# Optimization experiments

Measured on AMD Instinct MI355X. Metric: run time of the kernel, lower is better.

Reference implementation:

```python
import jax, jax.numpy as jnp
import numpy as np

N_NODES = 4096
EDGE_PROB = 0.01


def setup_inputs() -> dict:
    key = jax.random.key(0)
    kx, ka, kw = jax.random.split(key, 3)
    x = jax.random.normal(kx, (4, 32, N_NODES, 12), dtype=jnp.float32)
    u = jax.random.uniform(ka, (N_NODES, N_NODES), dtype=jnp.float32)
    adj = (u < EDGE_PROB).astype(jnp.float32)
    adj = jnp.maximum(adj, adj.T)
    weight = jax.random.normal(kw, (3, 32, 32), dtype=jnp.float32) * 0.1
    bias = jnp.zeros((32,), dtype=jnp.float32)
    return {"x": x, "adj": adj, "weight": weight, "bias": bias}


def reference(x, adj, weight, bias):
    # x: [B, c_in, N, T] -> [B, T, N, c_in] as in AdaptiveGraphConv.forward
    B, C, N, T = x.shape
    h = jnp.transpose(x, (0, 3, 2, 1))  # [B, T, N, C]
    # DenseChebConv (K=3): L = I - D^{-1/2} A D^{-1/2}, inf -> 0 for isolated nodes
    d = adj.sum(axis=-1)
    d_inv_sqrt = jnp.where(d > 0, jnp.where(d > 0, d, 1.0) ** -0.5, 0.0)
    norm_adj = d_inv_sqrt[:, None] * adj * d_inv_sqrt[None, :]
    L = jnp.eye(N, dtype=x.dtype) - norm_adj
    Tx0 = h
    Tx1 = jnp.einsum('mn,btnc->btmc', L, h)
    Tx2 = 2.0 * jnp.einsum('mn,btnc->btmc', L, Tx1) - Tx0
    out = (jnp.einsum('btnc,co->btno', Tx0, weight[0])
           + jnp.einsum('btnc,co->btno', Tx1, weight[1])
           + jnp.einsum('btnc,co->btno', Tx2, weight[2])
           + bias)
    # back to [B, c_out, N, T]
    return jnp.transpose(out, (0, 3, 2, 1))
```

## Files before the change

### kernel.cpp

```cpp
#include <hip/hip_runtime.h>

#define NN 4096
#define CC 32
#define TT 12
#define BB 4
#define BT 48
#define NC 1536
#define MAXD 192
#define FW 256
#define NCH 6
#define SOP 33

typedef float f32x4 __attribute__((ext_vector_type(4)));
typedef short short8 __attribute__((ext_vector_type(8)));

__device__ __forceinline__ float bf2f(unsigned short h) {
  return __uint_as_float(((unsigned int)h) << 16);
}
__device__ __forceinline__ unsigned short f2bf(float f) {
  unsigned int u = __float_as_uint(f);
  return (unsigned short)((u + 0x7FFFu + ((u >> 16) & 1u)) >> 16);
}
__device__ __forceinline__ float blo(unsigned int w) { return __uint_as_float(w << 16); }
__device__ __forceinline__ float bhi(unsigned int w) { return __uint_as_float(w & 0xFFFF0000u); }

__global__ void k_detect(const unsigned int* __restrict__ w, int* __restrict__ flag) {
  __shared__ int s;
  if (threadIdx.x == 0) s = 0;
  __syncthreads();
  int h = 0;
  for (int i = threadIdx.x; i < 256; i += 64) {
    unsigned int e = (w[i] >> 7) & 0xFFu;
    if (e >= 90u && e <= 141u) ++h;
  }
  atomicAdd(&s, h);
  __syncthreads();
  if (threadIdx.x == 0) *flag = (s >= 150) ? 1 : 0;
}

template<int BF16>
__global__ __launch_bounds__(256) void k_build(const void* __restrict__ adjv,
                                               uint2* __restrict__ edges,
                                               int* __restrict__ deg, float* __restrict__ dis,
                                               const int* __restrict__ flag) {
  if ((*flag != 0) != (BF16 != 0)) return;
  __shared__ int cnt;
  int m = blockIdx.x;
  if (threadIdx.x == 0) cnt = 0;
  __syncthreads();
  unsigned int* ecol = (unsigned int*)(edges + m * MAXD);
  if (BF16) {
    const uint4* row = (const uint4*)((const unsigned short*)adjv + (size_t)m * NN);
    for (int i = threadIdx.x; i < NN / 8; i += 256) {
      uint4 v = row[i];
      unsigned int ws[4] = {v.x, v.y, v.z, v.w};
      #pragma unroll
      for (int k = 0; k < 4; ++k) {
        if (ws[k] & 0xFFFFu) {
          int p = atomicAdd(&cnt, 1);
          if (p < MAXD) ecol[p * 2] = (unsigned int)(i * 8 + k * 2);
        }
        if (ws[k] >> 16) {
          int p = atomicAdd(&cnt, 1);
          if (p < MAXD) ecol[p * 2] = (unsigned int)(i * 8 + k * 2 + 1);
        }
      }
    }
  } else {
    const uint4* row = (const uint4*)((const float*)adjv + (size_t)m * NN);
    for (int i = threadIdx.x; i < NN / 4; i += 256) {
      uint4 v = row[i];
      unsigned int ws[4] = {v.x, v.y, v.z, v.w};
      #pragma unroll
      for (int k = 0; k < 4; ++k) {
        if (ws[k] != 0) {
          int p = atomicAdd(&cnt, 1);
          if (p < MAXD) ecol[p * 2] = (unsigned int)(i * 4 + k);
        }
      }
    }
  }
  __syncthreads();
  if (threadIdx.x == 0) {
    int d = cnt < MAXD ? cnt : MAXD;
    deg[m] = d;
    dis[m] = d > 0 ? (float)(1.0 / sqrt((double)d)) : 0.0f;
  }
}

__global__ __launch_bounds__(192) void k_wt(uint2* __restrict__ edges,
                                            const int* __restrict__ deg,
                                            const float* __restrict__ dis) {
  int m = blockIdx.x;
  int j = threadIdx.x;
  if (j < deg[m]) {
    unsigned int* e = (unsigned int*)(edges + m * MAXD + j);
    unsigned int col = e[0];
    e[1] = __float_as_uint(dis[col]);
  }
}

template<int BF16>
__global__ __launch_bounds__(256) void k_trans(const void* __restrict__ xv,
                                               unsigned short* __restrict__ H,
                                               const int* __restrict__ flag) {
  if ((*flag != 0) != (BF16 != 0)) return;
  int i = blockIdx.x * 256 + threadIdx.x;
  int c4 = (i & 7) << 2;
  int r  = i >> 3;
  int bt = r % BT;
  int b  = bt / TT;
  int t  = bt - b * TT;
  int n  = r / BT;
  const size_t S = (size_t)NN * TT;
  size_t src = ((((size_t)b * CC + c4) * NN + n) * TT + t);
  ushort4 v;
  if (BF16) {
    const unsigned short* x = (const unsigned short*)xv;
    v.x = x[src]; v.y = x[src + S]; v.z = x[src + 2 * S]; v.w = x[src + 3 * S];
  } else {
    const float* x = (const float*)xv;
    v.x = f2bf(x[src]); v.y = f2bf(x[src + S]);
    v.z = f2bf(x[src + 2 * S]); v.w = f2bf(x[src + 3 * S]);
  }
  *(ushort4*)(H + (size_t)r * CC + c4) = v;
}

__global__ __launch_bounds__(256) void k_gather1(const unsigned short* __restrict__ H,
                                                 const uint2* __restrict__ edges,
                                                 const int* __restrict__ deg,
                                                 const float* __restrict__ dis,
                                                 unsigned short* __restrict__ T1) {
  int wid = __builtin_amdgcn_readfirstlane(threadIdx.x >> 6);
  int lane = threadIdx.x & 63;
  int m = blockIdx.x * 4 + wid;
  int q = blockIdx.y;
  int d = deg[m];
  float dm = dis[m];
  const uint2* ep = edges + m * MAXD;
  int fo = q * FW + (lane << 2);
  const unsigned short* Hf = H + fo;
  float a0 = 0.f, a1 = 0.f, a2 = 0.f, a3 = 0.f;
  #pragma unroll 4
  for (int e = 0; e < d; ++e) {
    uint2 ew = ep[e];
    int cc = (int)ew.x;
    float w = __uint_as_float(ew.y);
    uint2 hv = *(const uint2*)(Hf + cc * NC);
    a0 = fmaf(w, blo(hv.x), a0);
    a1 = fmaf(w, bhi(hv.x), a1);
    a2 = fmaf(w, blo(hv.y), a2);
    a3 = fmaf(w, bhi(hv.y), a3);
  }
  uint2 hm = *(const uint2*)(Hf + m * NC);
  ushort4 o;
  o.x = f2bf(blo(hm.x) - dm * a0);
  o.y = f2bf(bhi(hm.x) - dm * a1);
  o.z = f2bf(blo(hm.y) - dm * a2);
  o.w = f2bf(bhi(hm.y) - dm * a3);
  *(ushort4*)(T1 + (size_t)m * NC + fo) = o;
}

__global__ __launch_bounds__(256) void k_gather2(const unsigned short* __restrict__ H,
                                                 const unsigned short* __restrict__ T1,
                                                 const uint2* __restrict__ edges,
                                                 const int* __restrict__ deg,
                                                 const float* __restrict__ dis,
                                                 unsigned short* __restrict__ T2) {
  int wid = __builtin_amdgcn_readfirstlane(threadIdx.x >> 6);
  int lane = threadIdx.x & 63;
  int m = blockIdx.x * 4 + wid;
  int q = blockIdx.y;
  int d = deg[m];
  float dm = dis[m];
  const uint2* ep = edges + m * MAXD;
  int fo = q * FW + (lane << 2);
  const unsigned short* Tf = T1 + fo;
  float a0 = 0.f, a1 = 0.f, a2 = 0.f, a3 = 0.f;
  #pragma unroll 4
  for (int e = 0; e < d; ++e) {
    uint2 ew = ep[e];
    int cc = (int)ew.x;
    float w = __uint_as_float(ew.y);
    uint2 hv = *(const uint2*)(Tf + cc * NC);
    a0 = fmaf(w, blo(hv.x), a0);
    a1 = fmaf(w, bhi(hv.x), a1);
    a2 = fmaf(w, blo(hv.y), a2);
    a3 = fmaf(w, bhi(hv.y), a3);
  }
  uint2 tm = *(const uint2*)(Tf + m * NC);
  uint2 hm = *(const uint2*)(H + (size_t)m * NC + fo);
  float td = 2.f * dm;
  ushort4 o;
  o.x = f2bf(2.f * blo(tm.x) - td * a0 - blo(hm.x));
  o.y = f2bf(2.f * bhi(tm.x) - td * a1 - bhi(hm.x));
  o.z = f2bf(2.f * blo(tm.y) - td * a2 - blo(hm.y));
  o.w = f2bf(2.f * bhi(tm.y) - td * a3 - bhi(hm.y));
  *(ushort4*)(T2 + (size_t)m * NC + fo) = o;
}

template<int BF16>
__global__ __launch_bounds__(256) void k_mix(const unsigned short* __restrict__ H,
                                             const unsigned short* __restrict__ T1,
                                             const unsigned short* __restrict__ T2,
                                             const void* __restrict__ wgtv,
                                             const void* __restrict__ biasv,
                                             void* __restrict__ outv,
                                             const int* __restrict__ flag) {
  if ((*flag != 0) != (BF16 != 0)) return;
  __shared__ __align__(16) float sOut[192 * SOP];
  int wid = threadIdx.x >> 6, lane = threadIdx.x & 63;
  int lm = lane & 15, quad = lane >> 4;
  short8 bhf[2][3], blf[2][3];
  for (int h = 0; h < 2; ++h) {
    for (int g = 0; g < 3; ++g) {
      short8 vh, vl;
      #pragma unroll
      for (int j = 0; j < 8; ++j) {
        int c = quad * 8 + j;
        int o = h * 16 + lm;
        float w = BF16 ? bf2f(((const unsigned short*)wgtv)[(g * CC + c) * CC + o])
                       : ((const float*)wgtv)[(g * CC + c) * CC + o];
        unsigned short hi = f2bf(w);
        float rem = w - bf2f(hi);
        vh[j] = (short)hi;
        vl[j] = (short)f2bf(rem);
      }
      bhf[h][g] = vh;
      blf[h][g] = vl;
    }
  }
  float bias0[2];
  #pragma unroll
  for (int h = 0; h < 2; ++h) {
    bias0[h] = BF16 ? bf2f(((const unsigned short*)biasv)[h * 16 + lm])
                    : ((const float*)biasv)[h * 16 + lm];
  }
  int n0 = blockIdx.x * 4;
  #pragma unroll
  for (int tI = 0; tI < 3; ++tI) {
    int r0l = wid * BT + tI * 16;
    size_t abase = ((size_t)(n0 * BT) + r0l + lm) * CC + quad * 8;
    short8 af0 = *(const short8*)(H + abase);
    short8 af1 = *(const short8*)(T1 + abase);
    short8 af2 = *(const short8*)(T2 + abase);
    #pragma unroll
    for (int h = 0; h < 2; ++h) {
      f32x4 acc = {bias0[h], bias0[h], bias0[h], bias0[h]};
      acc = __builtin_amdgcn_mfma_f32_16x16x32_bf16(af0, bhf[h][0], acc, 0, 0, 0);
      acc = __builtin_amdgcn_mfma_f32_16x16x32_bf16(af0, blf[h][0], acc, 0, 0, 0);
      acc = __builtin_amdgcn_mfma_f32_16x16x32_bf16(af1, bhf[h][1], acc, 0, 0, 0);
      acc = __builtin_amdgcn_mfma_f32_16x16x32_bf16(af1, blf[h][1], acc, 0, 0, 0);
      acc = __builtin_amdgcn_mfma_f32_16x16x32_bf16(af2, bhf[h][2], acc, 0, 0, 0);
      acc = __builtin_amdgcn_mfma_f32_16x16x32_bf16(af2, blf[h][2], acc, 0, 0, 0);
      int o = h * 16 + lm;
      #pragma unroll
      for (int reg = 0; reg < 4; ++reg) {
        sOut[(r0l + quad * 4 + reg) * SOP + o] = acc[reg];
      }
    }
  }
  __syncthreads();
  #pragma unroll
  for (int j = 0; j < 6; ++j) {
    int idx = j * 256 + threadIdx.x;
    int bo = idx / 12;
    int fq = idx - bo * 12;
    int b = bo >> 5, o = bo & 31;
    int p0 = fq * 4;
    float v[4];
    #pragma unroll
    for (int k = 0; k < 4; ++k) {
      int p = p0 + k;
      int nl = p / 12, t = p - nl * 12;
      v[k] = sOut[(nl * BT + b * TT + t) * SOP + o];
    }
    size_t base = (((size_t)bo * NN) + n0) * TT + p0;
    if (BF16) {
      ushort4 s = {f2bf(v[0]), f2bf(v[1]), f2bf(v[2]), f2bf(v[3])};
      *(ushort4*)((unsigned short*)outv + base) = s;
    } else {
      *(float4*)((float*)outv + base) = make_float4(v[0], v[1], v[2], v[3]);
    }
  }
}

extern "C" void kernel_launch(void* const* d_in, const int* in_sizes, int n_in,
                              void* d_out, int out_size, void* d_ws, size_t ws_size,
                              hipStream_t stream) {
  const void* x    = d_in[0];
  const void* adj  = d_in[1];
  const void* wgt  = d_in[2];
  const void* bias = d_in[3];
  char* ws = (char*)d_ws;
  int*   flag = (int*)ws;
  float* dis  = (float*)(ws + 256);
  int*   deg  = (int*)(ws + 256 + 16384);
  uint2* edges = (uint2*)(ws + 256 + 32768);
  char* p = ws + 256 + 32768 + (size_t)NN * MAXD * 8;
  unsigned short* H  = (unsigned short*)p;
  unsigned short* T1 = (unsigned short*)(p + (size_t)NN * NC * 2);
  unsigned short* T2 = (unsigned short*)(p + (size_t)NN * NC * 4);

  k_detect<<<1, 64, 0, stream>>>((const unsigned int*)wgt, flag);
  k_build<1><<<NN, 256, 0, stream>>>(adj, edges, deg, dis, flag);
  k_build<0><<<NN, 256, 0, stream>>>(adj, edges, deg, dis, flag);
  k_wt<<<NN, 192, 0, stream>>>(edges, deg, dis);
  k_trans<1><<<(NN * BT * 8) / 256, 256, 0, stream>>>(x, H, flag);
  k_trans<0><<<(NN * BT * 8) / 256, 256, 0, stream>>>(x, H, flag);
  k_gather1<<<dim3(NN / 4, NCH), 256, 0, stream>>>(H, edges, deg, dis, T1);
  k_gather2<<<dim3(NN / 4, NCH), 256, 0, stream>>>(H, T1, edges, deg, dis, T2);
  k_mix<1><<<NN / 4, 256, 0, stream>>>(H, T1, T2, wgt, bias, d_out, flag);
  k_mix<0><<<NN / 4, 256, 0, stream>>>(H, T1, T2, wgt, bias, d_out, flag);
}
```

Baseline: 285.9 us.

## Inline dtype sniffing, tile transpose via LDS, widen gather vectors, pad edge lists

Removes the separate dtype-detect kernel and the duplicated templated launches by having each kernel sniff the weight dtype itself. The input transpose is reworked to use an LDS tile, so global reads are coalesced vector loads instead of strided scalar ones. The gathers now load 8 bf16 per lane (16-byte loads) with half as many feature chunks. Edge lists are padded to a multiple of 8 with zero-weight self edges so the unrolled loop has no remainder. The cost is redundant sniffing work in every block and more registers per thread in the gathers.

```diff
diff --git a/kernel.cpp b/kernel.cpp
--- a/kernel.cpp
+++ b/kernel.cpp
@@ -7,9 +7,9 @@
 #define BT 48
 #define NC 1536
 #define MAXD 192
-#define FW 256
-#define NCH 6
-#define SOP 33
+#define FWW 512
+#define NCH 3
+#define STP 36
 
 typedef float f32x4 __attribute__((ext_vector_type(4)));
 typedef short short8 __attribute__((ext_vector_type(8)));
@@ -24,32 +24,28 @@
 __device__ __forceinline__ float blo(unsigned int w) { return __uint_as_float(w << 16); }
 __device__ __forceinline__ float bhi(unsigned int w) { return __uint_as_float(w & 0xFFFF0000u); }
 
-__global__ void k_detect(const unsigned int* __restrict__ w, int* __restrict__ flag) {
-  __shared__ int s;
-  if (threadIdx.x == 0) s = 0;
-  __syncthreads();
-  int h = 0;
-  for (int i = threadIdx.x; i < 256; i += 64) {
-    unsigned int e = (w[i] >> 7) & 0xFFu;
-    if (e >= 90u && e <= 141u) ++h;
-  }
-  atomicAdd(&s, h);
-  __syncthreads();
-  if (threadIdx.x == 0) *flag = (s >= 150) ? 1 : 0;
-}
-
-template<int BF16>
+__device__ __forceinline__ int sniff_bf16(const void* w) {
+  const unsigned int* p = (const unsigned int*)w;
+  int hits = 0;
+  #pragma unroll 8
+  for (int i = 0; i < 256; ++i) {
+    unsigned int e = (p[i] >> 7) & 0xFFu;
+    hits += (e >= 90u && e <= 141u) ? 1 : 0;
+  }
+  return hits >= 150;
+}
+
 __global__ __launch_bounds__(256) void k_build(const void* __restrict__ adjv,
+                                               const void* __restrict__ wgtv,
                                                uint2* __restrict__ edges,
-                                               int* __restrict__ deg, float* __restrict__ dis,
-                                               const int* __restrict__ flag) {
-  if ((*flag != 0) != (BF16 != 0)) return;
+                                               int* __restrict__ deg, float* __restrict__ dis) {
+  int bf16 = sniff_bf16(wgtv);
   __shared__ int cnt;
   int m = blockIdx.x;
   if (threadIdx.x == 0) cnt = 0;
   __syncthreads();
   unsigned int* ecol = (unsigned int*)(edges + m * MAXD);
-  if (BF16) {
+  if (bf16) {
     const uint4* row = (const uint4*)((const unsigned short*)adjv + (size_t)m * NN);
     for (int i = threadIdx.x; i < NN / 8; i += 256) {
       uint4 v = row[i];
@@ -89,41 +85,56 @@
 }
 
 __global__ __launch_bounds__(192) void k_wt(uint2* __restrict__ edges,
-                                            const int* __restrict__ deg,
+                                            int* __restrict__ deg,
                                             const float* __restrict__ dis) {
   int m = blockIdx.x;
   int j = threadIdx.x;
-  if (j < deg[m]) {
+  int d = deg[m];
+  int dp = (d + 7) & ~7;
+  if (j < d) {
     unsigned int* e = (unsigned int*)(edges + m * MAXD + j);
-    unsigned int col = e[0];
-    e[1] = __float_as_uint(dis[col]);
-  }
-}
-
-template<int BF16>
+    e[1] = __float_as_uint(dis[e[0]]);
+  } else if (j < dp) {
+    edges[m * MAXD + j] = make_uint2((unsigned int)m, 0u);
+  }
+  if (j == 0) deg[m] = dp;
+}
+
 __global__ __launch_bounds__(256) void k_trans(const void* __restrict__ xv,
-                                               unsigned short* __restrict__ H,
-                                               const int* __restrict__ flag) {
-  if ((*flag != 0) != (BF16 != 0)) return;
-  int i = blockIdx.x * 256 + threadIdx.x;
-  int c4 = (i & 7) << 2;
-  int r  = i >> 3;
-  int bt = r % BT;
-  int b  = bt / TT;
-  int t  = bt - b * TT;
-  int n  = r / BT;
-  const size_t S = (size_t)NN * TT;
-  size_t src = ((((size_t)b * CC + c4) * NN + n) * TT + t);
-  ushort4 v;
-  if (BF16) {
-    const unsigned short* x = (const unsigned short*)xv;
-    v.x = x[src]; v.y = x[src + S]; v.z = x[src + 2 * S]; v.w = x[src + 3 * S];
-  } else {
-    const float* x = (const float*)xv;
-    v.x = f2bf(x[src]); v.y = f2bf(x[src + S]);
-    v.z = f2bf(x[src + 2 * S]); v.w = f2bf(x[src + 3 * S]);
-  }
-  *(ushort4*)(H + (size_t)r * CC + c4) = v;
+                                               const void* __restrict__ wgtv,
+                                               unsigned short* __restrict__ H) {
+  __shared__ unsigned short sT[768 * STP];
+  int bf16 = sniff_bf16(wgtv);
+  int b = blockIdx.x >> 6;
+  int n0 = (blockIdx.x & 63) * 64;
+  int c = threadIdx.x >> 3;
+  int l8 = threadIdx.x & 7;
+  size_t base = ((size_t)(b * CC + c) * NN + n0) * TT;
+  #pragma unroll
+  for (int it = 0; it < 24; ++it) {
+    int j0 = l8 * 4 + it * 32;
+    ushort4 v;
+    if (bf16) {
+      v = *(const ushort4*)((const unsigned short*)xv + base + j0);
+    } else {
+      float4 f = *(const float4*)((const float*)xv + base + j0);
+      v.x = f2bf(f.x); v.y = f2bf(f.y); v.z = f2bf(f.z); v.w = f2bf(f.w);
+    }
+    sT[(j0 + 0) * STP + c] = v.x;
+    sT[(j0 + 1) * STP + c] = v.y;
+    sT[(j0 + 2) * STP + c] = v.z;
+    sT[(j0 + 3) * STP + c] = v.w;
+  }
+  __syncthreads();
+  int inner = threadIdx.x & 7;
+  #pragma unroll
+  for (int k = 0; k < 24; ++k) {
+    int p = (threadIdx.x >> 3) + 32 * k;
+    int nl = p / TT, t = p - nl * TT;
+    ushort4 v = *(const ushort4*)&sT[p * STP + inner * 4];
+    size_t off = ((size_t)(n0 + nl) * BT + b * TT + t) * CC + inner * 4;
+    *(ushort4*)(H + off) = v;
+  }
 }
 
 __global__ __launch_bounds__(256) void k_gather1(const unsigned short* __restrict__ H,
@@ -134,31 +145,32 @@
   int wid = __builtin_amdgcn_readfirstlane(threadIdx.x >> 6);
   int lane = threadIdx.x & 63;
   int m = blockIdx.x * 4 + wid;
-  int q = blockIdx.y;
   int d = deg[m];
   float dm = dis[m];
   const uint2* ep = edges + m * MAXD;
-  int fo = q * FW + (lane << 2);
+  int fo = blockIdx.y * FWW + lane * 8;
   const unsigned short* Hf = H + fo;
-  float a0 = 0.f, a1 = 0.f, a2 = 0.f, a3 = 0.f;
-  #pragma unroll 4
+  float a0 = 0.f, a1 = 0.f, a2 = 0.f, a3 = 0.f, a4 = 0.f, a5 = 0.f, a6 = 0.f, a7 = 0.f;
+  #pragma unroll 8
   for (int e = 0; e < d; ++e) {
     uint2 ew = ep[e];
     int cc = (int)ew.x;
     float w = __uint_as_float(ew.y);
-    uint2 hv = *(const uint2*)(Hf + cc * NC);
-    a0 = fmaf(w, blo(hv.x), a0);
-    a1 = fmaf(w, bhi(hv.x), a1);
-    a2 = fmaf(w, blo(hv.y), a2);
-    a3 = fmaf(w, bhi(hv.y), a3);
-  }
-  uint2 hm = *(const uint2*)(Hf + m * NC);
-  ushort4 o;
-  o.x = f2bf(blo(hm.x) - dm * a0);
-  o.y = f2bf(bhi(hm.x) - dm * a1);
-  o.z = f2bf(blo(hm.y) - dm * a2);
-  o.w = f2bf(bhi(hm.y) - dm * a3);
-  *(ushort4*)(T1 + (size_t)m * NC + fo) = o;
+    uint4 hv = *(const uint4*)(Hf + cc * NC);
+    a0 = fmaf(w, blo(hv.x), a0); a1 = fmaf(w, bhi(hv.x), a1);
+    a2 = fmaf(w, blo(hv.y), a2); a3 = fmaf(w, bhi(hv.y), a3);
+    a4 = fmaf(w, blo(hv.z), a4); a5 = fmaf(w, bhi(hv.z), a5);
+    a6 = fmaf(w, blo(hv.w), a6); a7 = fmaf(w, bhi(hv.w), a7);
+  }
+  uint4 hm = *(const uint4*)(Hf + m * NC);
+  ushort4 o0, o1;
+  o0.x = f2bf(blo(hm.x) - dm * a0); o0.y = f2bf(bhi(hm.x) - dm * a1);
+  o0.z = f2bf(blo(hm.y) - dm * a2); o0.w = f2bf(bhi(hm.y) - dm * a3);
+  o1.x = f2bf(blo(hm.z) - dm * a4); o1.y = f2bf(bhi(hm.z) - dm * a5);
+  o1.z = f2bf(blo(hm.w) - dm * a6); o1.w = f2bf(bhi(hm.w) - dm * a7);
+  unsigned short* op = T1 + (size_t)m * NC + fo;
+  *(ushort4*)op = o0;
+  *(ushort4*)(op + 4) = o1;
 }
 
 __global__ __launch_bounds__(256) void k_gather2(const unsigned short* __restrict__ H,
@@ -170,71 +182,83 @@
   int wid = __builtin_amdgcn_readfirstlane(threadIdx.x >> 6);
   int lane = threadIdx.x & 63;
   int m = blockIdx.x * 4 + wid;
-  int q = blockIdx.y;
   int d = deg[m];
   float dm = dis[m];
   const uint2* ep = edges + m * MAXD;
-  int fo = q * FW + (lane << 2);
+  int fo = blockIdx.y * FWW + lane * 8;
   const unsigned short* Tf = T1 + fo;
-  float a0 = 0.f, a1 = 0.f, a2 = 0.f, a3 = 0.f;
-  #pragma unroll 4
+  float a0 = 0.f, a1 = 0.f, a2 = 0.f, a3 = 0.f, a4 = 0.f, a5 = 0.f, a6 = 0.f, a7 = 0.f;
+  #pragma unroll 8
   for (int e = 0; e < d; ++e) {
     uint2 ew = ep[e];
     int cc = (int)ew.x;
     float w = __uint_as_float(ew.y);
-    uint2 hv = *(const uint2*)(Tf + cc * NC);
-    a0 = fmaf(w, blo(hv.x), a0);
-    a1 = fmaf(w, bhi(hv.x), a1);
-    a2 = fmaf(w, blo(hv.y), a2);
-    a3 = fmaf(w, bhi(hv.y), a3);
-  }
-  uint2 tm = *(const uint2*)(Tf + m * NC);
-  uint2 hm = *(const uint2*)(H + (size_t)m * NC + fo);
+    uint4 hv = *(const uint4*)(Tf + cc * NC);
+    a0 = fmaf(w, blo(hv.x), a0); a1 = fmaf(w, bhi(hv.x), a1);
+    a2 = fmaf(w, blo(hv.y), a2); a3 = fmaf(w, bhi(hv.y), a3);
+    a4 = fmaf(w, blo(hv.z), a4); a5 = fmaf(w, bhi(hv.z), a5);
+    a6 = fmaf(w, blo(hv.w), a6); a7 = fmaf(w, bhi(hv.w), a7);
+  }
+  uint4 tm = *(const uint4*)(Tf + m * NC);
+  uint4 hm = *(const uint4*)(H + (size_t)m * NC + fo);
   float td = 2.f * dm;
-  ushort4 o;
-  o.x = f2bf(2.f * blo(tm.x) - td * a0 - blo(hm.x));
-  o.y = f2bf(2.f * bhi(tm.x) - td * a1 - bhi(hm.x));
-  o.z = f2bf(2.f * blo(tm.y) - td * a2 - blo(hm.y));
-  o.w = f2bf(2.f * bhi(tm.y) - td * a3 - bhi(hm.y));
-  *(ushort4*)(T2 + (size_t)m * NC + fo) = o;
-}
-
-template<int BF16>
+  ushort4 o0, o1;
+  o0.x = f2bf(2.f * blo(tm.x) - td * a0 - blo(hm.x));
+  o0.y = f2bf(2.f * bhi(tm.x) - td * a1 - bhi(hm.x));
+  o0.z = f2bf(2.f * blo(tm.y) - td * a2 - blo(hm.y));
+  o0.w = f2bf(2.f * bhi(tm.y) - td * a3 - bhi(hm.y));
+  o1.x = f2bf(2.f * blo(tm.z) - td * a4 - blo(hm.z));
+  o1.y = f2bf(2.f * bhi(tm.z) - td * a5 - bhi(hm.z));
+  o1.z = f2bf(2.f * blo(tm.w) - td * a6 - blo(hm.w));
+  o1.w = f2bf(2.f * bhi(tm.w) - td * a7 - bhi(hm.w));
+  unsigned short* op = T2 + (size_t)m * NC + fo;
+  *(ushort4*)op = o0;
+  *(ushort4*)(op + 4) = o1;
+}
+
+#define SOP 33
 __global__ __launch_bounds__(256) void k_mix(const unsigned short* __restrict__ H,
                                              const unsigned short* __restrict__ T1,
                                              const unsigned short* __restrict__ T2,
                                              const void* __restrict__ wgtv,
                                              const void* __restrict__ biasv,
-                                             void* __restrict__ outv,
-                                             const int* __restrict__ flag) {
-  if ((*flag != 0) != (BF16 != 0)) return;
+                                             void* __restrict__ outv) {
+  int bf16 = sniff_bf16(wgtv);
   __shared__ __align__(16) float sOut[192 * SOP];
   int wid = threadIdx.x >> 6, lane = threadIdx.x & 63;
   int lm = lane & 15, quad = lane >> 4;
   short8 bhf[2][3], blf[2][3];
-  for (int h = 0; h < 2; ++h) {
-    for (int g = 0; g < 3; ++g) {
-      short8 vh, vl;
-      #pragma unroll
-      for (int j = 0; j < 8; ++j) {
-        int c = quad * 8 + j;
-        int o = h * 16 + lm;
-        float w = BF16 ? bf2f(((const unsigned short*)wgtv)[(g * CC + c) * CC + o])
-                       : ((const float*)wgtv)[(g * CC + c) * CC + o];
-        unsigned short hi = f2bf(w);
-        float rem = w - bf2f(hi);
-        vh[j] = (short)hi;
-        vl[j] = (short)f2bf(rem);
+  float bias0[2];
+  if (bf16) {
+    const unsigned short* W = (const unsigned short*)wgtv;
+    for (int h = 0; h < 2; ++h)
+      for (int g = 0; g < 3; ++g) {
+        short8 vh, vl;
+        #pragma unroll
+        for (int j = 0; j < 8; ++j) {
+          float w = bf2f(W[(g * CC + quad * 8 + j) * CC + h * 16 + lm]);
+          unsigned short hi = f2bf(w);
+          vh[j] = (short)hi;
+          vl[j] = (short)f2bf(w - bf2f(hi));
+        }
+        bhf[h][g] = vh; blf[h][g] = vl;
       }
-      bhf[h][g] = vh;
-      blf[h][g] = vl;
-    }
-  }
-  float bias0[2];
-  #pragma unroll
-  for (int h = 0; h < 2; ++h) {
-    bias0[h] = BF16 ? bf2f(((const unsigned short*)biasv)[h * 16 + lm])
-                    : ((const float*)biasv)[h * 16 + lm];
+    for (int h = 0; h < 2; ++h) bias0[h] = bf2f(((const unsigned short*)biasv)[h * 16 + lm]);
+  } else {
+    const float* W = (const float*)wgtv;
+    for (int h = 0; h < 2; ++h)
+      for (int g = 0; g < 3; ++g) {
+        short8 vh, vl;
+        #pragma unroll
+        for (int j = 0; j < 8; ++j) {
+          float w = W[(g * CC + quad * 8 + j) * CC + h * 16 + lm];
+          unsigned short hi = f2bf(w);
+          vh[j] = (short)hi;
+          vl[j] = (short)f2bf(w - bf2f(hi));
+        }
+        bhf[h][g] = vh; blf[h][g] = vl;
+      }
+    for (int h = 0; h < 2; ++h) bias0[h] = ((const float*)biasv)[h * 16 + lm];
   }
   int n0 = blockIdx.x * 4;
   #pragma unroll
@@ -255,9 +279,8 @@
       acc = __builtin_amdgcn_mfma_f32_16x16x32_bf16(af2, blf[h][2], acc, 0, 0, 0);
       int o = h * 16 + lm;
       #pragma unroll
-      for (int reg = 0; reg < 4; ++reg) {
+      for (int reg = 0; reg < 4; ++reg)
         sOut[(r0l + quad * 4 + reg) * SOP + o] = acc[reg];
-      }
     }
   }
   __syncthreads();
@@ -272,11 +295,11 @@
     #pragma unroll
     for (int k = 0; k < 4; ++k) {
       int p = p0 + k;
-      int nl = p / 12, t = p - nl * 12;
+      int nl = p / TT, t = p - nl * TT;
       v[k] = sOut[(nl * BT + b * TT + t) * SOP + o];
     }
     size_t base = (((size_t)bo * NN) + n0) * TT + p0;
-    if (BF16) {
+    if (bf16) {
       ushort4 s = {f2bf(v[0]), f2bf(v[1]), f2bf(v[2]), f2bf(v[3])};
       *(ushort4*)((unsigned short*)outv + base) = s;
     } else {
@@ -293,23 +316,18 @@
   const void* wgt  = d_in[2];
   const void* bias = d_in[3];
   char* ws = (char*)d_ws;
-  int*   flag = (int*)ws;
-  float* dis  = (float*)(ws + 256);
-  int*   deg  = (int*)(ws + 256 + 16384);
-  uint2* edges = (uint2*)(ws + 256 + 32768);
-  char* p = ws + 256 + 32768 + (size_t)NN * MAXD * 8;
+  float* dis  = (float*)ws;
+  int*   deg  = (int*)(ws + 16384);
+  uint2* edges = (uint2*)(ws + 32768);
+  char* p = ws + 32768 + (size_t)NN * MAXD * 8;
   unsigned short* H  = (unsigned short*)p;
   unsigned short* T1 = (unsigned short*)(p + (size_t)NN * NC * 2);
   unsigned short* T2 = (unsigned short*)(p + (size_t)NN * NC * 4);
 
-  k_detect<<<1, 64, 0, stream>>>((const unsigned int*)wgt, flag);
-  k_build<1><<<NN, 256, 0, stream>>>(adj, edges, deg, dis, flag);
-  k_build<0><<<NN, 256, 0, stream>>>(adj, edges, deg, dis, flag);
+  k_build<<<NN, 256, 0, stream>>>(adj, wgt, edges, deg, dis);
   k_wt<<<NN, 192, 0, stream>>>(edges, deg, dis);
-  k_trans<1><<<(NN * BT * 8) / 256, 256, 0, stream>>>(x, H, flag);
-  k_trans<0><<<(NN * BT * 8) / 256, 256, 0, stream>>>(x, H, flag);
+  k_trans<<<256, 256, 0, stream>>>(x, wgt, H);
   k_gather1<<<dim3(NN / 4, NCH), 256, 0, stream>>>(H, edges, deg, dis, T1);
   k_gather2<<<dim3(NN / 4, NCH), 256, 0, stream>>>(H, T1, edges, deg, dis, T2);
-  k_mix<1><<<NN / 4, 256, 0, stream>>>(H, T1, T2, wgt, bias, d_out, flag);
-  k_mix<0><<<NN / 4, 256, 0, stream>>>(H, T1, T2, wgt, bias, d_out, flag);
-}
+  k_mix<<<NN / 4, 256, 0, stream>>>(H, T1, T2, wgt, bias, d_out);
+}
```

New measurement: 295.7 us. +3.4%, slower.
